# Optimization experiments

Measured on AMD Instinct MI355X. Metric: run time of the kernel, lower is better.

## Reference

```python
import jax, jax.numpy as jnp
import numpy as np

N_NODES = 100000
N_EDGES = 1600000
IN_C = 128
HID = 128
OUT_C = 10
NUM_GRAPHS = 512


def _glorot(key, shape):
    lim = float(np.sqrt(6.0 / (shape[0] + shape[1])))
    return jax.random.uniform(key, shape, jnp.float32, -lim, lim)


def setup_inputs() -> dict:
    key = jax.random.key(0)
    ks = jax.random.split(key, 12)
    x = jax.random.normal(ks[0], (N_NODES, IN_C), jnp.float32)
    edge_index = jax.random.randint(ks[1], (2, N_EDGES), 0, N_NODES, jnp.int64)
    batch = jnp.sort(jax.random.randint(ks[2], (N_NODES,), 0, NUM_GRAPHS, jnp.int64))
    return {
        'x': x, 'edge_index': edge_index, 'batch': batch,
        'Wc0': _glorot(ks[3], (IN_C, HID)), 'bc0': jnp.zeros((HID,), jnp.float32),
        'Wc1': _glorot(ks[4], (HID, HID)), 'bc1': jnp.zeros((HID,), jnp.float32),
        'Wc2': _glorot(ks[5], (HID, HID)), 'bc2': jnp.zeros((HID,), jnp.float32),
        'W1': _glorot(ks[6], (HID, HID)), 'b1': jnp.zeros((HID,), jnp.float32),
        'W2': _glorot(ks[7], (HID, OUT_C)), 'b2': jnp.zeros((OUT_C,), jnp.float32),
    }


def _gcn_conv(x, src, dst, W, b, n):
    # PyG GCNConv: add self-loops, symmetric norm D^-1/2 (A+I) D^-1/2, then XW + b.
    # deg includes the self-loop (+1); messages flow src -> dst.
    deg = jax.ops.segment_sum(jnp.ones((src.shape[0],), x.dtype), dst, num_segments=n) + 1.0
    dinv = jax.lax.rsqrt(deg)  # deg >= 1 so no zeros
    h = x @ W  # [N, H]
    coef = dinv[src] * dinv[dst]  # [E]
    agg = jax.ops.segment_sum(h[src] * coef[:, None], dst, num_segments=n)
    agg = agg + h * (dinv * dinv)[:, None]  # self-loop contribution, no edge materialization
    return agg + b


def reference(x, edge_index, batch, Wc0, bc0, Wc1, bc1, Wc2, bc2, W1, b1, W2, b2):
    n = x.shape[0]
    src, dst = edge_index[0], edge_index[1]
    # eval mode: dropout is identity
    h = jax.nn.relu(_gcn_conv(x, src, dst, Wc0, bc0, n))
    h = jax.nn.relu(_gcn_conv(h, src, dst, Wc1, bc1, n))
    h = _gcn_conv(h, src, dst, Wc2, bc2, n)
    # global_mean_pool over graphs
    sums = jax.ops.segment_sum(h, batch, num_segments=NUM_GRAPHS)
    counts = jax.ops.segment_sum(jnp.ones((n,), h.dtype), batch, num_segments=NUM_GRAPHS)
    pooled = sums / jnp.maximum(counts, 1.0)[:, None]  # [G, H]
    out = jax.nn.relu(pooled @ W1 + b1)
    return out @ W2 + b2  # [G, OUT_C]
```

## Files before the change

### kernel.cpp

```cpp
#include <hip/hip_runtime.h>
#include <hip/hip_bf16.h>
#include <stdint.h>

#define HID     128
#define OUTC    10
#define NGRAPH  512
#define NGROUP  256
#define PSIZE   256
#define CAP     64
#define NBIN_MX 400

using bf16x8 = __attribute__((ext_vector_type(8))) short;
using f32x4  = __attribute__((ext_vector_type(4))) float;
using u32x4  = __attribute__((ext_vector_type(4))) uint32_t;

__device__ __forceinline__ short f2bf(float f) {
    __hip_bfloat16 h = __float2bfloat16(f);
    return *reinterpret_cast<short*>(&h);
}
__device__ __forceinline__ float bf2f(short s) {
    union { uint32_t u; float f; } x; x.u = ((uint32_t)(uint16_t)s) << 16; return x.f;
}
__device__ __forceinline__ float bflo(uint32_t v) {
    union { uint32_t u; float f; } x; x.u = v << 16; return x.f;
}
__device__ __forceinline__ float bfhi(uint32_t v) {
    union { uint32_t u; float f; } x; x.u = v & 0xffff0000u; return x.f;
}
__device__ __forceinline__ uint32_t pk2(float lo, float hi) {
    return (uint32_t)(uint16_t)f2bf(lo) | ((uint32_t)(uint16_t)f2bf(hi) << 16);
}

__device__ __forceinline__ int detect_f64(const int* __restrict__ ei) {
    int lane = threadIdx.x & 63;
    int v = ei[2 * lane + 1];
    unsigned long long b = __ballot(v == 0);
    return (b == ~0ULL) ? 1 : 0;
}

__device__ __forceinline__ int fetch_idx(const int* __restrict__ p, long j, int f64) {
    return p[f64 ? (j << 1) : j];
}

__global__ void __launch_bounds__(256) prep_kernel(
        const int* __restrict__ ei, const int* __restrict__ batch,
        const float* __restrict__ W0, const float* __restrict__ W1,
        const float* __restrict__ W2, short* __restrict__ Wt,
        int* __restrict__ gstart, int n) {
    __shared__ float Ws[64][129];
    int bid = blockIdx.x;
    const int tid = threadIdx.x;

    if (bid < 3) {
        const float* W = (bid == 0) ? W0 : (bid == 1) ? W1 : W2;
        short* hi = Wt + (size_t)bid * 2 * HID * HID;
        short* lo = hi + HID * HID;
        for (int half = 0; half < 2; ++half) {
            const int kbase = half * 64;
#pragma unroll
            for (int it = 0; it < 8; ++it) {
                int idx = (tid + it * 256) * 4;
                int k = idx >> 7, c = idx & 127;
                float4 v = *(const float4*)(W + (size_t)(kbase + k) * HID + c);
                Ws[k][c] = v.x; Ws[k][c + 1] = v.y; Ws[k][c + 2] = v.z; Ws[k][c + 3] = v.w;
            }
            __syncthreads();
            const int k2 = tid & 63;
            const int cb = tid >> 6;
#pragma unroll
            for (int it = 0; it < 32; ++it) {
                int c = cb + it * 4;
                float w = Ws[k2][c];
                short h = f2bf(w);
                hi[(size_t)c * HID + kbase + k2] = h;
                lo[(size_t)c * HID + kbase + k2] = f2bf(w - bf2f(h));
            }
            __syncthreads();
        }
        return;
    }
    bid -= 3;
    const int f = detect_f64(ei);
    int i = bid * 256 + tid;
    if (i >= n) return;
    int b  = fetch_idx(batch, i, f);
    int bp = (i == 0) ? -1 : fetch_idx(batch, i - 1, f);
    for (int g = bp + 1; g <= b; ++g) gstart[g] = i;
    if (i == n - 1) {
        for (int g = b + 1; g <= NGRAPH; ++g) gstart[g] = n;
    }
}

__global__ void __launch_bounds__(512) bin_scatter_kernel(
        const int* __restrict__ ei, int* __restrict__ cnt,
        uint32_t* __restrict__ binned, long E, int NBIN) {
    __shared__ int      lcnt[NBIN_MX];
    __shared__ uint32_t lbin[NBIN_MX * CAP];
    const int g   = blockIdx.x;
    const int tid = threadIdx.x;
    const int f   = detect_f64(ei);
    for (int b = tid; b < NBIN; b += 512) lcnt[b] = 0;
    __syncthreads();
    const long chunk = (E + gridDim.x - 1) / gridDim.x;
    const long e0 = (long)g * chunk;
    const long e1 = (e0 + chunk < E) ? e0 + chunk : E;
    for (long e = e0 + tid; e < e1; e += 512) {
        int s = fetch_idx(ei, e, f);
        int d = fetch_idx(ei, E + e, f);
        int b = d >> 8;
        int p = atomicAdd(&lcnt[b], 1);
        if (p < CAP)
            lbin[b * CAP + p] = (uint32_t)s | ((uint32_t)(d & (PSIZE - 1)) << 20);
    }
    __syncthreads();
    const int wv = tid >> 6, lane = tid & 63;
    for (int b = wv; b < NBIN; b += 8) {
        int c = min(lcnt[b], CAP);
        uint32_t* __restrict__ dst = binned + ((size_t)b * NGROUP + g) * CAP;
        for (int i = lane; i < c; i += 64) dst[i] = lbin[b * CAP + i];
        if (lane == 0) cnt[b * NGROUP + g] = c;
    }
}

__global__ void __launch_bounds__(1024) binscan_kernel(
        const int* __restrict__ cnt, int* __restrict__ bofs, int NBIN) {
    __shared__ int stot[NBIN_MX];
    __shared__ int wsum[16];
    const int tid  = threadIdx.x;
    const int lane = tid & 63;
    const int wid  = tid >> 6;
    for (int b = wid; b < NBIN; b += 16) {
        int s = 0;
#pragma unroll
        for (int i = 0; i < NGROUP / 64; ++i) s += cnt[b * NGROUP + lane + i * 64];
#pragma unroll
        for (int d = 1; d < 64; d <<= 1) s += __shfl_xor(s, d, 64);
        if (lane == 0) stot[b] = s;
    }
    __syncthreads();
    int v = (tid < NBIN) ? stot[tid] : 0;
    int inc = v;
#pragma unroll
    for (int d = 1; d < 64; d <<= 1) {
        int t = __shfl_up(inc, d, 64);
        if (lane >= d) inc += t;
    }
    if (lane == 63) wsum[wid] = inc;
    __syncthreads();
    if (wid == 0) {
        int ws = (lane < 16) ? wsum[lane] : 0;
        int winc = ws;
#pragma unroll
        for (int d = 1; d < 16; d <<= 1) {
            int t = __shfl_up(winc, d, 64);
            if (lane >= d) winc += t;
        }
        if (lane < 16) wsum[lane] = winc - ws;
    }
    __syncthreads();
    int excl = wsum[wid] + (inc - v);
    if (tid <= NBIN) bofs[tid] = excl;
}

__global__ void __launch_bounds__(512) bin_build_kernel(
        const uint32_t* __restrict__ binned, const int* __restrict__ cnt,
        const int* __restrict__ bofs, int* __restrict__ ofs,
        float* __restrict__ dinv, int* __restrict__ col,
        int n, int NBIN, long E) {
    __shared__ int lcnt[PSIZE];
    __shared__ int lofs[PSIZE];
    __shared__ int lrank[PSIZE];
    __shared__ int wtot[4];
    const int b    = blockIdx.x;
    const int v0   = b * PSIZE;
    const int nn   = min(PSIZE, n - v0);
    const int tid  = threadIdx.x;
    const int wv   = tid >> 6;
    const int lane = tid & 63;
    if (tid < PSIZE) { lcnt[tid] = 0; lrank[tid] = 0; }
    __syncthreads();
    for (int sg = wv; sg < NGROUP; sg += 8) {
        const int c = min(cnt[b * NGROUP + sg], CAP);
        const uint32_t* __restrict__ src = binned + ((size_t)b * NGROUP + sg) * CAP;
        for (int i = lane; i < c; i += 64)
            atomicAdd(&lcnt[src[i] >> 20], 1);
    }
    __syncthreads();
    if (tid < PSIZE) {
        int v = lcnt[tid];
        int inc = v;
#pragma unroll
        for (int d = 1; d < 64; d <<= 1) {
            int t = __shfl_up(inc, d, 64);
            if (lane >= d) inc += t;
        }
        if (lane == 63) wtot[wv] = inc;
        lofs[tid] = inc - v;
    }
    __syncthreads();
    if (tid < PSIZE) {
        int add = 0;
#pragma unroll
        for (int k = 0; k < 4; ++k) if (k < wv) add += wtot[k];
        lofs[tid] += add;
    }
    __syncthreads();
    const int base = bofs[b];
    for (int sg = wv; sg < NGROUP; sg += 8) {
        const int c = min(cnt[b * NGROUP + sg], CAP);
        const uint32_t* __restrict__ src = binned + ((size_t)b * NGROUP + sg) * CAP;
        for (int i = lane; i < c; i += 64) {
            uint32_t v = src[i];
            int dl = (int)(v >> 20);
            int rk = atomicAdd(&lrank[dl], 1);
            col[base + lofs[dl] + rk] = (int)(v & 0xFFFFFu);
        }
    }
    if (tid < nn) {
        ofs[v0 + tid]  = base + lofs[tid];
        dinv[v0 + tid] = rsqrtf((float)lcnt[tid] + 1.0f);
    }
    if (tid == 0 && v0 + nn == n) ofs[n] = (int)E;
}

template<bool AFP32>
__global__ void __launch_bounds__(256) gemm_hs_kernel(
        const void* __restrict__ Ap, const short* __restrict__ Wt,
        const float* __restrict__ dinv, short* __restrict__ hs, int n) {
    __shared__ __attribute__((aligned(16))) short As[128 * 128];
    const short* __restrict__ Bh = Wt;
    const short* __restrict__ Bl = Wt + HID * HID;
    const int tid = threadIdx.x;
    const int w  = tid >> 6;
    const int l  = tid & 63;
    const int lr = l & 15;
    const int kq = l >> 4;
    const int r0 = blockIdx.x * 128;

    const float* Af = (const float*)Ap;
    const short* Ab = (const short*)Ap;

#pragma unroll
    for (int it = 0; it < 8; ++it) {
        int ci  = tid + it * 256;
        int row = ci >> 4, c = ci & 15;
        int rg  = r0 + row; if (rg >= n) rg = n - 1;
        bf16x8 tv;
        if (AFP32) {
            const float* ap = Af + (size_t)rg * HID + c * 8;
            float4 f0 = *(const float4*)ap;
            float4 f1 = *(const float4*)(ap + 4);
            tv[0] = f2bf(f0.x); tv[1] = f2bf(f0.y); tv[2] = f2bf(f0.z); tv[3] = f2bf(f0.w);
            tv[4] = f2bf(f1.x); tv[5] = f2bf(f1.y); tv[6] = f2bf(f1.z); tv[7] = f2bf(f1.w);
        } else {
            tv = *(const bf16x8*)(Ab + (size_t)rg * HID + c * 8);
        }
        *(bf16x8*)(As + row * 128 + ((c ^ (row & 15)) << 3)) = tv;
    }
    __syncthreads();

    f32x4 acc[8][2] = {};
    const int col0 = w * 32 + lr;
    const int col1 = w * 32 + 16 + lr;

#pragma unroll
    for (int ks = 0; ks < 4; ++ks) {
        const int k0 = ks * 32 + kq * 8;
        bf16x8 a[8];
#pragma unroll
        for (int rf = 0; rf < 8; ++rf) {
            int row = rf * 16 + lr;
            a[rf] = *(const bf16x8*)(As + row * 128 + (((ks * 4 + kq) ^ lr) << 3));
        }
        bf16x8 bh0 = *(const bf16x8*)(Bh + (size_t)col0 * HID + k0);
        bf16x8 bh1 = *(const bf16x8*)(Bh + (size_t)col1 * HID + k0);
        bf16x8 bl0 = *(const bf16x8*)(Bl + (size_t)col0 * HID + k0);
        bf16x8 bl1 = *(const bf16x8*)(Bl + (size_t)col1 * HID + k0);
#pragma unroll
        for (int rf = 0; rf < 8; ++rf) {
            acc[rf][0] = __builtin_amdgcn_mfma_f32_16x16x32_bf16(a[rf], bh0, acc[rf][0], 0, 0, 0);
            acc[rf][1] = __builtin_amdgcn_mfma_f32_16x16x32_bf16(a[rf], bh1, acc[rf][1], 0, 0, 0);
            acc[rf][0] = __builtin_amdgcn_mfma_f32_16x16x32_bf16(a[rf], bl0, acc[rf][0], 0, 0, 0);
            acc[rf][1] = __builtin_amdgcn_mfma_f32_16x16x32_bf16(a[rf], bl1, acc[rf][1], 0, 0, 0);
        }
    }
#pragma unroll
    for (int rf = 0; rf < 8; ++rf) {
#pragma unroll
        for (int rg = 0; rg < 4; ++rg) {
            int row = r0 + rf * 16 + kq * 4 + rg;
            if (row < n) {
                float dn = dinv[row];
                hs[(size_t)row * HID + col0] = f2bf(acc[rf][0][rg] * dn);
                hs[(size_t)row * HID + col1] = f2bf(acc[rf][1][rg] * dn);
            }
        }
    }
}

__device__ __forceinline__ void acc_add(float* acc, u32x4 v) {
    acc[0] += bflo(v.x); acc[1] += bfhi(v.x);
    acc[2] += bflo(v.y); acc[3] += bfhi(v.y);
    acc[4] += bflo(v.z); acc[5] += bfhi(v.z);
    acc[6] += bflo(v.w); acc[7] += bfhi(v.w);
}

__global__ void __launch_bounds__(256) agg_kernel(
        const short* __restrict__ hs, const float* __restrict__ dinv,
        const int* __restrict__ ofs, const int* __restrict__ col,
        const float* __restrict__ bias, short* __restrict__ out,
        int n, int do_relu) {
    int node = blockIdx.x * 4 + (threadIdx.x >> 6);
    if (node >= n) return;
    const int lane = threadIdx.x & 63;
    const int g    = lane >> 4;
    const int sub  = lane & 15;
    const u32x4* __restrict__ rows = (const u32x4*)hs;

    float acc[8] = {0.f, 0.f, 0.f, 0.f, 0.f, 0.f, 0.f, 0.f};
    if (g == 0) {
        u32x4 sv = rows[(size_t)node * 16 + sub];
        acc_add(acc, sv);
    }
    const int e0 = ofs[node], e1 = ofs[node + 1];
    int e = e0;
    for (; e + 16 <= e1; e += 16) {
        int c0 = col[e + g];
        int c1 = col[e + 4 + g];
        int c2 = col[e + 8 + g];
        int c3 = col[e + 12 + g];
        u32x4 v0 = rows[(size_t)c0 * 16 + sub];
        u32x4 v1 = rows[(size_t)c1 * 16 + sub];
        u32x4 v2 = rows[(size_t)c2 * 16 + sub];
        u32x4 v3 = rows[(size_t)c3 * 16 + sub];
        acc_add(acc, v0); acc_add(acc, v1); acc_add(acc, v2); acc_add(acc, v3);
    }
    for (; e + 4 <= e1; e += 4) {
        int c0 = col[e + g];
        u32x4 v0 = rows[(size_t)c0 * 16 + sub];
        acc_add(acc, v0);
    }
    if (e + g < e1) {
        int c0 = col[e + g];
        u32x4 v0 = rows[(size_t)c0 * 16 + sub];
        acc_add(acc, v0);
    }
#pragma unroll
    for (int i = 0; i < 8; ++i) {
        acc[i] += __shfl_xor(acc[i], 16, 64);
        acc[i] += __shfl_xor(acc[i], 32, 64);
    }
    if (g == 0) {
        const float dn = dinv[node];
        float4 b0 = *(const float4*)(bias + 8 * sub);
        float4 b1 = *(const float4*)(bias + 8 * sub + 4);
        float o0 = fmaf(acc[0], dn, b0.x);
        float o1 = fmaf(acc[1], dn, b0.y);
        float o2 = fmaf(acc[2], dn, b0.z);
        float o3 = fmaf(acc[3], dn, b0.w);
        float o4 = fmaf(acc[4], dn, b1.x);
        float o5 = fmaf(acc[5], dn, b1.y);
        float o6 = fmaf(acc[6], dn, b1.z);
        float o7 = fmaf(acc[7], dn, b1.w);
        if (do_relu) {
            o0 = fmaxf(o0, 0.f); o1 = fmaxf(o1, 0.f);
            o2 = fmaxf(o2, 0.f); o3 = fmaxf(o3, 0.f);
            o4 = fmaxf(o4, 0.f); o5 = fmaxf(o5, 0.f);
            o6 = fmaxf(o6, 0.f); o7 = fmaxf(o7, 0.f);
        }
        u32x4 pk;
        pk.x = pk2(o0, o1); pk.y = pk2(o2, o3);
        pk.z = pk2(o4, o5); pk.w = pk2(o6, o7);
        ((u32x4*)out)[(size_t)node * 16 + sub] = pk;
    }
}

__global__ void __launch_bounds__(128) pool_mlp_kernel(
        const short* __restrict__ h, const int* __restrict__ gstart,
        const float* __restrict__ W1, const float* __restrict__ b1,
        const float* __restrict__ W2, const float* __restrict__ b2,
        float* __restrict__ out) {
    __shared__ float p[HID];
    __shared__ float hid[HID];
    int g = blockIdx.x, c = threadIdx.x;
    int s = gstart[g], e = gstart[g + 1];
    float acc = 0.f;
    int i = s;
    for (; i + 4 <= e; i += 4) {
        acc += bf2f(h[(size_t)i * HID + c]) + bf2f(h[(size_t)(i + 1) * HID + c])
             + bf2f(h[(size_t)(i + 2) * HID + c]) + bf2f(h[(size_t)(i + 3) * HID + c]);
    }
    for (; i < e; ++i) acc += bf2f(h[(size_t)i * HID + c]);
    p[c] = acc / fmaxf((float)(e - s), 1.f);
    __syncthreads();
    float a = b1[c];
#pragma unroll 8
    for (int k = 0; k < HID; ++k) a = fmaf(p[k], W1[k * HID + c], a);
    hid[c] = fmaxf(a, 0.f);
    __syncthreads();
    if (c < OUTC) {
        float o = b2[c];
#pragma unroll 8
        for (int k = 0; k < HID; ++k) o = fmaf(hid[k], W2[k * OUTC + c], o);
        out[g * OUTC + c] = o;
    }
}

extern "C" void kernel_launch(void* const* d_in, const int* in_sizes, int n_in,
                              void* d_out, int out_size, void* d_ws, size_t ws_size,
                              hipStream_t stream) {
    const float* x   = (const float*)d_in[0];
    const int*   ei  = (const int*)d_in[1];
    const int*   bat = (const int*)d_in[2];
    const float* Wc0 = (const float*)d_in[3];
    const float* bc0 = (const float*)d_in[4];
    const float* Wc1 = (const float*)d_in[5];
    const float* bc1 = (const float*)d_in[6];
    const float* Wc2 = (const float*)d_in[7];
    const float* bc2 = (const float*)d_in[8];
    const float* W1  = (const float*)d_in[9];
    const float* b1  = (const float*)d_in[10];
    const float* W2  = (const float*)d_in[11];
    const float* b2  = (const float*)d_in[12];
    float* out = (float*)d_out;

    const int  n = in_sizes[0] / HID;
    const long E = in_sizes[1] / 2;
    const int  NBIN = (n + PSIZE - 1) / PSIZE;

    char* w = (char*)d_ws;
    size_t off = 0;
    auto carve = [&](size_t bytes) {
        void* p = w + off;
        off += (bytes + 255) & ~(size_t)255;
        return p;
    };
    int*   cnt     = (int*)carve((size_t)NBIN * NGROUP * 4);
    int*   bofs    = (int*)carve((size_t)(NBIN + 1) * 4);
    int*   ofs     = (int*)carve((size_t)(n + 1) * 4);
    float* dinv    = (float*)carve((size_t)n * 4);
    int*   gstart  = (int*)carve((NGRAPH + 1) * 4);
    int*   col     = (int*)carve((size_t)E * 4);
    short* Wt      = (short*)carve((size_t)3 * 2 * HID * HID * 2);
    uint32_t* binned = (uint32_t*)carve((size_t)NBIN * NGROUP * CAP * 4);
    short* hs      = (short*)carve((size_t)n * HID * 2);
    short* h       = (short*)carve((size_t)n * HID * 2);

    const int nbb = (n + 255) / 256;
    prep_kernel<<<3 + nbb, 256, 0, stream>>>(ei, bat, Wc0, Wc1, Wc2, Wt, gstart, n);

    bin_scatter_kernel<<<NGROUP, 512, 0, stream>>>(ei, cnt, binned, E, NBIN);
    binscan_kernel<<<1, 1024, 0, stream>>>(cnt, bofs, NBIN);
    bin_build_kernel<<<NBIN, 512, 0, stream>>>(binned, cnt, bofs, ofs, dinv, col,
                                               n, NBIN, E);

    const int gb = (n + 127) / 128;
    const int ab = (n + 3) / 4;
    const size_t WSTRIDE = (size_t)2 * HID * HID;
    gemm_hs_kernel<true><<<gb, 256, 0, stream>>>(x, Wt, dinv, hs, n);
    agg_kernel<<<ab, 256, 0, stream>>>(hs, dinv, ofs, col, bc0, h, n, 1);
    gemm_hs_kernel<false><<<gb, 256, 0, stream>>>(h, Wt + WSTRIDE, dinv, hs, n);
    agg_kernel<<<ab, 256, 0, stream>>>(hs, dinv, ofs, col, bc1, h, n, 1);
    gemm_hs_kernel<false><<<gb, 256, 0, stream>>>(h, Wt + 2 * WSTRIDE, dinv, hs, n);
    agg_kernel<<<ab, 256, 0, stream>>>(hs, dinv, ofs, col, bc2, h, n, 0);

    pool_mlp_kernel<<<NGRAPH, 128, 0, stream>>>(h, gstart, W1, b1, W2, b2, out);
}
```

Before: 375.9 us.

## Fuse prep and edge binning into one front kernel; load GEMM tiles direct-to-LDS

The weight-transpose/split, graph-start computation and edge bin scatter now run in a single 512-thread launch instead of two, which removes one kernel launch and its tail. In the bf16-input GEMM, the A tile is loaded with global_load_lds straight into LDS. That load reads the XOR-swizzled column from global memory so the shared-memory layout stays the same without a register round trip. The fused kernel's larger shared-memory footprint caps residency, and the weight-prep blocks now share a launch shape with the binning blocks.

```diff
diff --git a/kernel.cpp b/kernel.cpp
--- a/kernel.cpp
+++ b/kernel.cpp
@@ -42,12 +42,15 @@
     return p[f64 ? (j << 1) : j];
 }
 
-__global__ void __launch_bounds__(256) prep_kernel(
+__global__ void __launch_bounds__(512) front_kernel(
         const int* __restrict__ ei, const int* __restrict__ batch,
         const float* __restrict__ W0, const float* __restrict__ W1,
         const float* __restrict__ W2, short* __restrict__ Wt,
-        int* __restrict__ gstart, int n) {
-    __shared__ float Ws[64][129];
+        int* __restrict__ cnt, uint32_t* __restrict__ binned,
+        int* __restrict__ gstart, int n, long E, int NBIN) {
+    __shared__ int      lcnt[NBIN_MX];
+    __shared__ uint32_t lbin[NBIN_MX * CAP];
+    __shared__ float    Ws[64][129];
     int bid = blockIdx.x;
     const int tid = threadIdx.x;
 
@@ -58,8 +61,8 @@
         for (int half = 0; half < 2; ++half) {
             const int kbase = half * 64;
 #pragma unroll
-            for (int it = 0; it < 8; ++it) {
-                int idx = (tid + it * 256) * 4;
+            for (int it = 0; it < 4; ++it) {
+                int idx = (tid + it * 512) * 4;
                 int k = idx >> 7, c = idx & 127;
                 float4 v = *(const float4*)(W + (size_t)(kbase + k) * HID + c);
                 Ws[k][c] = v.x; Ws[k][c + 1] = v.y; Ws[k][c + 2] = v.z; Ws[k][c + 3] = v.w;
@@ -68,40 +71,33 @@
             const int k2 = tid & 63;
             const int cb = tid >> 6;
 #pragma unroll
-            for (int it = 0; it < 32; ++it) {
-                int c = cb + it * 4;
-                float w = Ws[k2][c];
-                short h = f2bf(w);
+            for (int it = 0; it < 16; ++it) {
+                int c = cb + it * 8;
+                float w0 = Ws[k2][c];
+                short h = f2bf(w0);
                 hi[(size_t)c * HID + kbase + k2] = h;
-                lo[(size_t)c * HID + kbase + k2] = f2bf(w - bf2f(h));
+                lo[(size_t)c * HID + kbase + k2] = f2bf(w0 - bf2f(h));
             }
             __syncthreads();
         }
         return;
     }
-    bid -= 3;
+    const int g = bid - 3;
     const int f = detect_f64(ei);
-    int i = bid * 256 + tid;
-    if (i >= n) return;
-    int b  = fetch_idx(batch, i, f);
-    int bp = (i == 0) ? -1 : fetch_idx(batch, i - 1, f);
-    for (int g = bp + 1; g <= b; ++g) gstart[g] = i;
-    if (i == n - 1) {
-        for (int g = b + 1; g <= NGRAPH; ++g) gstart[g] = n;
-    }
-}
-
-__global__ void __launch_bounds__(512) bin_scatter_kernel(
-        const int* __restrict__ ei, int* __restrict__ cnt,
-        uint32_t* __restrict__ binned, long E, int NBIN) {
-    __shared__ int      lcnt[NBIN_MX];
-    __shared__ uint32_t lbin[NBIN_MX * CAP];
-    const int g   = blockIdx.x;
-    const int tid = threadIdx.x;
-    const int f   = detect_f64(ei);
+    {
+        int i = g * 512 + tid;
+        if (i < n) {
+            int b  = fetch_idx(batch, i, f);
+            int bp = (i == 0) ? -1 : fetch_idx(batch, i - 1, f);
+            for (int gg = bp + 1; gg <= b; ++gg) gstart[gg] = i;
+            if (i == n - 1) {
+                for (int gg = b + 1; gg <= NGRAPH; ++gg) gstart[gg] = n;
+            }
+        }
+    }
     for (int b = tid; b < NBIN; b += 512) lcnt[b] = 0;
     __syncthreads();
-    const long chunk = (E + gridDim.x - 1) / gridDim.x;
+    const long chunk = (E + NGROUP - 1) / NGROUP;
     const long e0 = (long)g * chunk;
     const long e1 = (e0 + chunk < E) ? e0 + chunk : E;
     for (long e = e0 + tid; e < e1; e += 512) {
@@ -240,22 +236,44 @@
     const float* Af = (const float*)Ap;
     const short* Ab = (const short*)Ap;
 
-#pragma unroll
-    for (int it = 0; it < 8; ++it) {
-        int ci  = tid + it * 256;
-        int row = ci >> 4, c = ci & 15;
-        int rg  = r0 + row; if (rg >= n) rg = n - 1;
-        bf16x8 tv;
-        if (AFP32) {
+    if (AFP32) {
+#pragma unroll
+        for (int it = 0; it < 8; ++it) {
+            int ci  = tid + it * 256;
+            int row = ci >> 4, c = ci & 15;
+            int rg  = r0 + row; if (rg >= n) rg = n - 1;
             const float* ap = Af + (size_t)rg * HID + c * 8;
             float4 f0 = *(const float4*)ap;
             float4 f1 = *(const float4*)(ap + 4);
+            bf16x8 tv;
             tv[0] = f2bf(f0.x); tv[1] = f2bf(f0.y); tv[2] = f2bf(f0.z); tv[3] = f2bf(f0.w);
             tv[4] = f2bf(f1.x); tv[5] = f2bf(f1.y); tv[6] = f2bf(f1.z); tv[7] = f2bf(f1.w);
-        } else {
-            tv = *(const bf16x8*)(Ab + (size_t)rg * HID + c * 8);
-        }
-        *(bf16x8*)(As + row * 128 + ((c ^ (row & 15)) << 3)) = tv;
+            *(bf16x8*)(As + row * 128 + ((c ^ (row & 15)) << 3)) = tv;
+        }
+    } else {
+#if __has_builtin(__builtin_amdgcn_global_load_lds)
+#pragma unroll
+        for (int it = 0; it < 8; ++it) {
+            int ci  = tid + it * 256;
+            int row = ci >> 4, c = ci & 15;
+            int rg  = r0 + row; if (rg >= n) rg = n - 1;
+            const short* gsrc = Ab + (size_t)rg * HID + ((c ^ (row & 15)) << 3);
+            short* ldst = As + (size_t)((tid & ~63) + it * 256) * 8;
+            __builtin_amdgcn_global_load_lds(
+                (const __attribute__((address_space(1))) uint32_t*)gsrc,
+                (__attribute__((address_space(3))) uint32_t*)ldst,
+                16, 0, 0);
+        }
+#else
+#pragma unroll
+        for (int it = 0; it < 8; ++it) {
+            int ci  = tid + it * 256;
+            int row = ci >> 4, c = ci & 15;
+            int rg  = r0 + row; if (rg >= n) rg = n - 1;
+            bf16x8 tv = *(const bf16x8*)(Ab + (size_t)rg * HID + c * 8);
+            *(bf16x8*)(As + row * 128 + ((c ^ (row & 15)) << 3)) = tv;
+        }
+#endif
     }
     __syncthreads();
 
@@ -446,10 +464,8 @@
     short* hs      = (short*)carve((size_t)n * HID * 2);
     short* h       = (short*)carve((size_t)n * HID * 2);
 
-    const int nbb = (n + 255) / 256;
-    prep_kernel<<<3 + nbb, 256, 0, stream>>>(ei, bat, Wc0, Wc1, Wc2, Wt, gstart, n);
-
-    bin_scatter_kernel<<<NGROUP, 512, 0, stream>>>(ei, cnt, binned, E, NBIN);
+    front_kernel<<<3 + NGROUP, 512, 0, stream>>>(ei, bat, Wc0, Wc1, Wc2, Wt,
+                                                 cnt, binned, gstart, n, E, NBIN);
     binscan_kernel<<<1, 1024, 0, stream>>>(cnt, bofs, NBIN);
     bin_build_kernel<<<NBIN, 512, 0, stream>>>(binned, cnt, bofs, ofs, dinv, col,
                                                n, NBIN, E);
```

New measurement: 374.9 us. No clear change (-0.3%).
